# Performance work log

Hardware: AMD Instinct MI355X
Metric: run time of the kernel (lower is better)

The kernel has to match this reference:

```python
import jax, jax.numpy as jnp
import numpy as np

B, T, C = 4, 4096, 512
H, KS = 8, 9
D = C // H
PAD = KS // 2


def setup_inputs() -> dict:
    key = jax.random.key(0)
    ks = jax.random.split(key, 9)
    s = 1.0 / np.sqrt(C)
    return {
        "x": jax.random.normal(ks[0], (B, T, C), jnp.float32),
        "Wq": jax.random.normal(ks[1], (C, C), jnp.float32) * s,
        "bq": jax.random.normal(ks[2], (C,), jnp.float32) * 0.01,
        "Wk": jax.random.normal(ks[3], (C, C), jnp.float32) * s,
        "bk": jax.random.normal(ks[4], (C,), jnp.float32) * 0.01,
        "Wv": jax.random.normal(ks[5], (C, C), jnp.float32) * s,
        "bv": jax.random.normal(ks[6], (C,), jnp.float32) * 0.01,
        "Wo": jax.random.normal(ks[7], (C, C), jnp.float32) * s,
        "bo": jax.random.normal(ks[8], (C,), jnp.float32) * 0.01,
    }


def reference(x, Wq, bq, Wk, bk, Wv, bv, Wo, bo):
    Bx, Tx, Cx = x.shape
    # projections (torch Linear: x @ W.T + b), split heads -> (B,H,T,D)
    q = (x @ Wq.T + bq).reshape(Bx, Tx, H, D).transpose(0, 2, 1, 3)
    k = (x @ Wk.T + bk).reshape(Bx, Tx, H, D).transpose(0, 2, 1, 3)
    v = (x @ Wv.T + bv).reshape(Bx, Tx, H, D).transpose(0, 2, 1, 3)
    # replicate-pad along time (matches F.pad mode='replicate')
    k_pad = jnp.pad(k, ((0, 0), (0, 0), (PAD, PAD), (0, 0)), mode='edge')
    v_pad = jnp.pad(v, ((0, 0), (0, 0), (PAD, PAD), (0, 0)), mode='edge')
    # window gather indices: (T, KS) into padded time axis
    idx = jnp.arange(Tx)[:, None] + jnp.arange(KS)[None, :]
    k_unf = k_pad[:, :, idx, :]  # (B,H,T,KS,D)
    v_unf = v_pad[:, :, idx, :]  # (B,H,T,KS,D)
    scale = 1.0 / np.sqrt(D)
    scores = jnp.einsum('bhtd,bhtkd->bhtk', q, k_unf) * scale  # (B,H,T,KS)
    attn = jax.nn.softmax(scores, axis=-1)
    y = jnp.einsum('bhtk,bhtkd->bhtd', attn, v_unf)  # (B,H,T,D)
    y = y.transpose(0, 2, 1, 3).reshape(Bx, Tx, Cx)
    return y @ Wo.T + bo
```

## Files before the change

kernel.cpp:

```cpp
#include <hip/hip_runtime.h>
#include <hip/hip_bf16.h>

#define B_    4
#define T_    4096
#define C_    512
#define H_    8
#define D_    64
#define KS_   9
#define PAD_  4
#define MTOT  (B_ * T_)
#define PLANE (MTOT * C_)
#define WU    (C_ * C_ / 8)

typedef __bf16 bf16_t;
typedef __bf16 bf16x8 __attribute__((ext_vector_type(8)));
typedef float  f32x4  __attribute__((ext_vector_type(4)));

__global__ __launch_bounds__(256)
void conv_all(const float* __restrict__ Wq, const float* __restrict__ Wk,
              const float* __restrict__ Wv, const float* __restrict__ Wo,
              const float* __restrict__ x,
              bf16_t* __restrict__ Wb, bf16_t* __restrict__ xb) {
  int i = blockIdx.x * 256 + threadIdx.x;
  const float* src;
  bf16_t* dst;
  if (i < 4 * WU) {
    int w = i >> 15;
    const float* W = (w == 0) ? Wq : (w == 1) ? Wk : (w == 2) ? Wv : Wo;
    src = W + (size_t)(i & (WU - 1)) * 8;
    dst = Wb + (size_t)i * 8;
  } else {
    size_t j = (size_t)(i - 4 * WU);
    src = x + j * 8;
    dst = xb + j * 8;
  }
  float4 f0 = ((const float4*)src)[0];
  float4 f1 = ((const float4*)src)[1];
  bf16x8 o;
  o[0] = (bf16_t)f0.x; o[1] = (bf16_t)f0.y; o[2] = (bf16_t)f0.z; o[3] = (bf16_t)f0.w;
  o[4] = (bf16_t)f1.x; o[5] = (bf16_t)f1.y; o[6] = (bf16_t)f1.z; o[7] = (bf16_t)f1.w;
  *(bf16x8*)dst = o;
}

#define BM   256
#define BN   128
#define BK   64
#define NKT  (C_ / BK)
#define ASL  (BM * BK)
#define BSL  (BN * BK)
#define SLOT (ASL + BSL)

#define GLD(srcp, off) __builtin_amdgcn_global_load_lds(                     \
    (const __attribute__((address_space(1))) unsigned int*)(srcp),           \
    (__attribute__((address_space(3))) unsigned int*)(&sm[off]), 16, 0, 0)

template<int MODE>
__global__ __launch_bounds__(512, 2)
void gemm8p(const bf16_t* __restrict__ A, const bf16_t* __restrict__ Bw,
            const float* __restrict__ b0, const float* __restrict__ b1,
            const float* __restrict__ b2, void* __restrict__ Outp) {
  __shared__ __align__(16) bf16_t sm[3 * SLOT];

  constexpr int GX  = (MODE == 0) ? (3 * C_ / BN) : (C_ / BN);
  constexpr int NWG = GX * (MTOT / BM);
  constexpr int CPX = NWG / 8;

  const int ord = blockIdx.y * GX + blockIdx.x;
  const int lg  = (ord & 7) * CPX + (ord >> 3);
  const int n0  = (lg % GX) * BN;
  const int m0  = (lg / GX) * BM;

  const int tid  = threadIdx.x;
  const int lane = tid & 63;
  const int wave = tid >> 6;
  const int wm   = wave >> 1;
  const int wn   = wave & 1;

  const bf16_t* aSrc[4];
  const bf16_t* bSrc[2];
#pragma unroll
  for (int s = 0; s < 4; ++s) {
    int u = s * 512 + tid, r = u >> 3, ch = u & 7;
    int cs = (ch ^ (r & 7)) << 3;
    if constexpr (MODE == 0) {
      aSrc[s] = A + (size_t)(m0 + r) * C_ + cs;
    } else {
      int bb = m0 >> 12, t0 = m0 & (T_ - 1);
      aSrc[s] = A + ((size_t)bb * H_ * T_ + t0 + r) * D_ + cs;
    }
  }
#pragma unroll
  for (int s = 0; s < 2; ++s) {
    int u = s * 512 + tid, r = u >> 3, ch = u & 7;
    int cs = (ch ^ (r & 7)) << 3;
    bSrc[s] = Bw + (size_t)(n0 + r) * C_ + cs;
  }
  constexpr size_t ASTEP = (MODE == 0) ? (size_t)BK : (size_t)T_ * D_;

#pragma unroll
  for (int s = 0; s < 4; ++s) GLD(aSrc[s], (s * 512 + tid) * 8);
#pragma unroll
  for (int s = 0; s < 2; ++s) GLD(bSrc[s], ASL + (s * 512 + tid) * 8);
#pragma unroll
  for (int s = 0; s < 4; ++s) GLD(aSrc[s] + ASTEP, SLOT + (s * 512 + tid) * 8);
#pragma unroll
  for (int s = 0; s < 2; ++s) GLD(bSrc[s] + BK, SLOT + ASL + (s * 512 + tid) * 8);
  asm volatile("s_waitcnt vmcnt(6)" ::: "memory");
  __builtin_amdgcn_s_barrier();

  f32x4 acc[4][4] = {};
  const int lr  = lane & 15;
  const int lq  = lane >> 4;
  const int co0 = ((0 + lq) ^ (lane & 7)) << 3;
  const int co1 = ((4 + lq) ^ (lane & 7)) << 3;

  int rsl = 0;
  for (int kt = 0; kt < NKT; ++kt) {
    const bf16_t* arow = &sm[rsl * SLOT + (wm * 64 + lr) * 64];
    const bf16_t* brow = &sm[rsl * SLOT + ASL + (wn * 64 + lr) * 64];
    const int  wof = ((rsl == 0) ? 2 : rsl - 1) * SLOT;
    const bool st  = (kt + 2 < NKT);
    const size_t ka = (size_t)(kt + 2) * ASTEP;
    const size_t kb = (size_t)(kt + 2) * BK;

    bf16x8 af[4][2], bfr[4][2];

#pragma unroll
    for (int i = 0; i < 4; ++i) {
      af[i][0] = *(const bf16x8*)(arow + i * 1024 + co0);
      af[i][1] = *(const bf16x8*)(arow + i * 1024 + co1);
    }
#pragma unroll
    for (int j = 0; j < 2; ++j) {
      bfr[j][0] = *(const bf16x8*)(brow + j * 1024 + co0);
      bfr[j][1] = *(const bf16x8*)(brow + j * 1024 + co1);
    }
    if (st) {
      GLD(aSrc[0] + ka, wof + (0 * 512 + tid) * 8);
      GLD(aSrc[1] + ka, wof + (1 * 512 + tid) * 8);
      GLD(aSrc[2] + ka, wof + (2 * 512 + tid) * 8);
      GLD(aSrc[3] + ka, wof + (3 * 512 + tid) * 8);
    }
    __builtin_amdgcn_sched_barrier(0);
    __builtin_amdgcn_s_barrier();
    asm volatile("s_waitcnt lgkmcnt(0)" ::: "memory");
    __builtin_amdgcn_sched_barrier(0);
    __builtin_amdgcn_s_setprio(1);
#pragma unroll
    for (int i = 0; i < 4; ++i)
#pragma unroll
      for (int j = 0; j < 2; ++j)
#pragma unroll
        for (int kk = 0; kk < 2; ++kk)
          acc[i][j] = __builtin_amdgcn_mfma_f32_16x16x32_bf16(
              af[i][kk], bfr[j][kk], acc[i][j], 0, 0, 0);
    __builtin_amdgcn_s_setprio(0);
    __builtin_amdgcn_sched_barrier(0);
    __builtin_amdgcn_s_barrier();

#pragma unroll
    for (int j = 2; j < 4; ++j) {
      bfr[j][0] = *(const bf16x8*)(brow + j * 1024 + co0);
      bfr[j][1] = *(const bf16x8*)(brow + j * 1024 + co1);
    }
    if (st) {
      GLD(bSrc[0] + kb, wof + ASL + (0 * 512 + tid) * 8);
      GLD(bSrc[1] + kb, wof + ASL + (1 * 512 + tid) * 8);
    }
    __builtin_amdgcn_sched_barrier(0);
    __builtin_amdgcn_s_barrier();
    asm volatile("s_waitcnt lgkmcnt(0)" ::: "memory");
    __builtin_amdgcn_sched_barrier(0);
    __builtin_amdgcn_s_setprio(1);
#pragma unroll
    for (int i = 0; i < 4; ++i)
#pragma unroll
      for (int j = 2; j < 4; ++j)
#pragma unroll
        for (int kk = 0; kk < 2; ++kk)
          acc[i][j] = __builtin_amdgcn_mfma_f32_16x16x32_bf16(
              af[i][kk], bfr[j][kk], acc[i][j], 0, 0, 0);
    __builtin_amdgcn_s_setprio(0);
    __builtin_amdgcn_sched_barrier(0);
    if (kt < NKT - 2)       asm volatile("s_waitcnt vmcnt(6)" ::: "memory");
    else if (kt == NKT - 2) asm volatile("s_waitcnt vmcnt(0)" ::: "memory");
    __builtin_amdgcn_s_barrier();
    rsl = (rsl == 2) ? 0 : rsl + 1;
  }

  const int cn = lane & 15;
  const int rq = (lane >> 4) << 2;
  if constexpr (MODE == 0) {
    const int z  = n0 >> 9;
    const float* bias = (z == 0) ? b0 : (z == 1) ? b1 : b2;
    const int bb = m0 >> 12;
    const int t0 = m0 & (T_ - 1);
    bf16_t* plane = (bf16_t*)Outp + (size_t)z * PLANE;
#pragma unroll
    for (int j = 0; j < 4; ++j) {
      const int cc  = (n0 & (C_ - 1)) + wn * 64 + j * 16 + cn;
      const int hh  = cc >> 6, dd = cc & 63;
      const float bvv = bias[cc];
      bf16_t* hb = plane + ((size_t)(bb * H_ + hh) * T_) * D_ + dd;
#pragma unroll
      for (int i = 0; i < 4; ++i)
#pragma unroll
        for (int r = 0; r < 4; ++r) {
          const int t = t0 + wm * 64 + i * 16 + rq + r;
          hb[(size_t)t * D_] = (bf16_t)(acc[i][j][r] + bvv);
        }
    }
  } else {
    float* outp = (float*)Outp;
#pragma unroll
    for (int j = 0; j < 4; ++j) {
      const int n = n0 + wn * 64 + j * 16 + cn;
      const float bvv = b0[n];
#pragma unroll
      for (int i = 0; i < 4; ++i)
#pragma unroll
        for (int r = 0; r < 4; ++r) {
          const int m = m0 + wm * 64 + i * 16 + rq + r;
          outp[(size_t)m * C_ + n] = acc[i][j][r] + bvv;
        }
    }
  }
}

__global__ __launch_bounds__(256)
void attn_kernel(const bf16_t* __restrict__ qkv, bf16_t* __restrict__ y) {
  const int tid  = threadIdx.x;
  const int sub  = tid & 7;
  const int tl   = tid >> 3;
  const int t    = blockIdx.x * 32 + tl;
  const int h    = blockIdx.y;
  const int b    = blockIdx.z;

  const size_t pl = (size_t)(b * H_ + h) * T_ * D_;
  const bf16_t* q = qkv + pl;
  const bf16_t* k = qkv + (size_t)PLANE + pl;
  const bf16_t* v = qkv + (size_t)2 * PLANE + pl;
  const int c = sub * 8;

  int tj[KS_];
#pragma unroll
  for (int j = 0; j < KS_; ++j) {
    int tt = t - PAD_ + j;
    tj[j] = tt < 0 ? 0 : (tt >= T_ ? T_ - 1 : tt);
  }

  bf16x8 q8 = *(const bf16x8*)(q + (size_t)t * D_ + c);
  float qf[8];
#pragma unroll
  for (int e = 0; e < 8; ++e) qf[e] = (float)q8[e];

  float s[KS_];
#pragma unroll
  for (int j = 0; j < KS_; ++j) {
    bf16x8 k8 = *(const bf16x8*)(k + (size_t)tj[j] * D_ + c);
    float d0 = 0.f;
#pragma unroll
    for (int e = 0; e < 8; ++e) d0 += qf[e] * (float)k8[e];
    s[j] = d0;
  }

#pragma unroll
  for (int m = 1; m < 8; m <<= 1)
#pragma unroll
    for (int j = 0; j < KS_; ++j) s[j] += __shfl_xor(s[j], m, 8);

  float mx = s[0];
#pragma unroll
  for (int j = 1; j < KS_; ++j) mx = fmaxf(mx, s[j]);
  float w[KS_], sum = 0.f;
#pragma unroll
  for (int j = 0; j < KS_; ++j) {
    w[j] = __expf((s[j] - mx) * 0.125f);
    sum += w[j];
  }
  const float inv = 1.f / sum;
#pragma unroll
  for (int j = 0; j < KS_; ++j) w[j] *= inv;

  float o[8] = {0.f, 0.f, 0.f, 0.f, 0.f, 0.f, 0.f, 0.f};
#pragma unroll
  for (int j = 0; j < KS_; ++j) {
    bf16x8 v8 = *(const bf16x8*)(v + (size_t)tj[j] * D_ + c);
#pragma unroll
    for (int e = 0; e < 8; ++e) o[e] += w[j] * (float)v8[e];
  }
  bf16x8 o8;
#pragma unroll
  for (int e = 0; e < 8; ++e) o8[e] = (bf16_t)o[e];
  *(bf16x8*)(y + pl + (size_t)t * D_ + c) = o8;
}

extern "C" void kernel_launch(void* const* d_in, const int* in_sizes, int n_in,
                              void* d_out, int out_size, void* d_ws, size_t ws_size,
                              hipStream_t stream) {
  const float* x  = (const float*)d_in[0];
  const float* Wq = (const float*)d_in[1];
  const float* bq = (const float*)d_in[2];
  const float* Wk = (const float*)d_in[3];
  const float* bk = (const float*)d_in[4];
  const float* Wv = (const float*)d_in[5];
  const float* bv = (const float*)d_in[6];
  const float* Wo = (const float*)d_in[7];
  const float* bo = (const float*)d_in[8];
  float* out = (float*)d_out;

  bf16_t* Wb  = (bf16_t*)d_ws;
  bf16_t* xb  = Wb + (size_t)4 * C_ * C_;
  bf16_t* qkv = xb + (size_t)PLANE;
  bf16_t* y   = xb;

  conv_all<<<(4 * WU + PLANE / 8) / 256, 256, 0, stream>>>(Wq, Wk, Wv, Wo, x, Wb, xb);
  gemm8p<0><<<dim3(3 * C_ / BN, MTOT / BM), 512, 0, stream>>>(
      xb, Wb, bq, bk, bv, qkv);
  attn_kernel<<<dim3(T_ / 32, H_, B_), 256, 0, stream>>>(qkv, y);
  gemm8p<1><<<dim3(C_ / BN, MTOT / BM), 512, 0, stream>>>(
      y, Wb + (size_t)3 * C_ * C_, bo, nullptr, nullptr, out);
}
```

Baseline: 167.2 us.

## Load GEMM weight fragments directly into registers, bypassing LDS staging

```diff
diff --git a/kernel.cpp b/kernel.cpp
--- a/kernel.cpp
+++ b/kernel.cpp
@@ -47,8 +47,6 @@
 #define BK   64
 #define NKT  (C_ / BK)
 #define ASL  (BM * BK)
-#define BSL  (BN * BK)
-#define SLOT (ASL + BSL)
 
 #define GLD(srcp, off) __builtin_amdgcn_global_load_lds(                     \
     (const __attribute__((address_space(1))) unsigned int*)(srcp),           \
@@ -59,7 +57,7 @@
 void gemm8p(const bf16_t* __restrict__ A, const bf16_t* __restrict__ Bw,
             const float* __restrict__ b0, const float* __restrict__ b1,
             const float* __restrict__ b2, void* __restrict__ Outp) {
-  __shared__ __align__(16) bf16_t sm[3 * SLOT];
+  __shared__ __align__(16) bf16_t sm[3 * ASL];
 
   constexpr int GX  = (MODE == 0) ? (3 * C_ / BN) : (C_ / BN);
   constexpr int NWG = GX * (MTOT / BM);
@@ -75,9 +73,10 @@
   const int wave = tid >> 6;
   const int wm   = wave >> 1;
   const int wn   = wave & 1;
+  const int lr   = lane & 15;
+  const int lq   = lane >> 4;
 
   const bf16_t* aSrc[4];
-  const bf16_t* bSrc[2];
 #pragma unroll
   for (int s = 0; s < 4; ++s) {
     int u = s * 512 + tid, r = u >> 3, ch = u & 7;
@@ -89,103 +88,73 @@
       aSrc[s] = A + ((size_t)bb * H_ * T_ + t0 + r) * D_ + cs;
     }
   }
-#pragma unroll
-  for (int s = 0; s < 2; ++s) {
-    int u = s * 512 + tid, r = u >> 3, ch = u & 7;
-    int cs = (ch ^ (r & 7)) << 3;
-    bSrc[s] = Bw + (size_t)(n0 + r) * C_ + cs;
-  }
   constexpr size_t ASTEP = (MODE == 0) ? (size_t)BK : (size_t)T_ * D_;
 
+  const bf16_t* bBase[4];
+#pragma unroll
+  for (int j = 0; j < 4; ++j)
+    bBase[j] = Bw + (size_t)(n0 + wn * 64 + j * 16 + lr) * C_ + lq * 8;
+
 #pragma unroll
   for (int s = 0; s < 4; ++s) GLD(aSrc[s], (s * 512 + tid) * 8);
 #pragma unroll
-  for (int s = 0; s < 2; ++s) GLD(bSrc[s], ASL + (s * 512 + tid) * 8);
-#pragma unroll
-  for (int s = 0; s < 4; ++s) GLD(aSrc[s] + ASTEP, SLOT + (s * 512 + tid) * 8);
-#pragma unroll
-  for (int s = 0; s < 2; ++s) GLD(bSrc[s] + BK, SLOT + ASL + (s * 512 + tid) * 8);
-  asm volatile("s_waitcnt vmcnt(6)" ::: "memory");
+  for (int s = 0; s < 4; ++s) GLD(aSrc[s] + ASTEP, ASL + (s * 512 + tid) * 8);
+  bf16x8 bfr[2][4][2];
+#pragma unroll
+  for (int j = 0; j < 4; ++j) {
+    bfr[0][j][0] = *(const bf16x8*)(bBase[j]);
+    bfr[0][j][1] = *(const bf16x8*)(bBase[j] + 32);
+  }
+  asm volatile("s_waitcnt vmcnt(12)" ::: "memory");
   __builtin_amdgcn_s_barrier();
 
   f32x4 acc[4][4] = {};
-  const int lr  = lane & 15;
-  const int lq  = lane >> 4;
   const int co0 = ((0 + lq) ^ (lane & 7)) << 3;
   const int co1 = ((4 + lq) ^ (lane & 7)) << 3;
 
-  int rsl = 0;
+#pragma unroll
   for (int kt = 0; kt < NKT; ++kt) {
-    const bf16_t* arow = &sm[rsl * SLOT + (wm * 64 + lr) * 64];
-    const bf16_t* brow = &sm[rsl * SLOT + ASL + (wn * 64 + lr) * 64];
-    const int  wof = ((rsl == 0) ? 2 : rsl - 1) * SLOT;
-    const bool st  = (kt + 2 < NKT);
-    const size_t ka = (size_t)(kt + 2) * ASTEP;
-    const size_t kb = (size_t)(kt + 2) * BK;
-
-    bf16x8 af[4][2], bfr[4][2];
-
+    const int rsl = kt % 3;
+    const int wof = ((kt + 2) % 3) * ASL;
+    const bf16_t* arow = &sm[rsl * ASL + (wm * 64 + lr) * 64];
+
+    bf16x8 af[4][2];
 #pragma unroll
     for (int i = 0; i < 4; ++i) {
       af[i][0] = *(const bf16x8*)(arow + i * 1024 + co0);
       af[i][1] = *(const bf16x8*)(arow + i * 1024 + co1);
     }
-#pragma unroll
-    for (int j = 0; j < 2; ++j) {
-      bfr[j][0] = *(const bf16x8*)(brow + j * 1024 + co0);
-      bfr[j][1] = *(const bf16x8*)(brow + j * 1024 + co1);
-    }
-    if (st) {
-      GLD(aSrc[0] + ka, wof + (0 * 512 + tid) * 8);
-      GLD(aSrc[1] + ka, wof + (1 * 512 + tid) * 8);
-      GLD(aSrc[2] + ka, wof + (2 * 512 + tid) * 8);
-      GLD(aSrc[3] + ka, wof + (3 * 512 + tid) * 8);
+    if (kt + 2 < NKT) {
+#pragma unroll
+      for (int s = 0; s < 4; ++s)
+        GLD(aSrc[s] + (size_t)(kt + 2) * ASTEP, wof + (s * 512 + tid) * 8);
+    }
+    if (kt + 1 < NKT) {
+#pragma unroll
+      for (int j = 0; j < 4; ++j) {
+        bfr[(kt + 1) & 1][j][0] =
+            *(const bf16x8*)(bBase[j] + (kt + 1) * 64);
+        bfr[(kt + 1) & 1][j][1] =
+            *(const bf16x8*)(bBase[j] + (kt + 1) * 64 + 32);
+      }
     }
     __builtin_amdgcn_sched_barrier(0);
-    __builtin_amdgcn_s_barrier();
     asm volatile("s_waitcnt lgkmcnt(0)" ::: "memory");
     __builtin_amdgcn_sched_barrier(0);
     __builtin_amdgcn_s_setprio(1);
 #pragma unroll
     for (int i = 0; i < 4; ++i)
 #pragma unroll
-      for (int j = 0; j < 2; ++j)
+      for (int j = 0; j < 4; ++j)
 #pragma unroll
         for (int kk = 0; kk < 2; ++kk)
           acc[i][j] = __builtin_amdgcn_mfma_f32_16x16x32_bf16(
-              af[i][kk], bfr[j][kk], acc[i][j], 0, 0, 0);
+              af[i][kk], bfr[kt & 1][j][kk], acc[i][j], 0, 0, 0);
     __builtin_amdgcn_s_setprio(0);
     __builtin_amdgcn_sched_barrier(0);
-    __builtin_amdgcn_s_barrier();
-
-#pragma unroll
-    for (int j = 2; j < 4; ++j) {
-      bfr[j][0] = *(const bf16x8*)(brow + j * 1024 + co0);
-      bfr[j][1] = *(const bf16x8*)(brow + j * 1024 + co1);
-    }
-    if (st) {
-      GLD(bSrc[0] + kb, wof + ASL + (0 * 512 + tid) * 8);
-      GLD(bSrc[1] + kb, wof + ASL + (1 * 512 + tid) * 8);
-    }
-    __builtin_amdgcn_sched_barrier(0);
-    __builtin_amdgcn_s_barrier();
-    asm volatile("s_waitcnt lgkmcnt(0)" ::: "memory");
-    __builtin_amdgcn_sched_barrier(0);
-    __builtin_amdgcn_s_setprio(1);
-#pragma unroll
-    for (int i = 0; i < 4; ++i)
-#pragma unroll
-      for (int j = 2; j < 4; ++j)
-#pragma unroll
-        for (int kk = 0; kk < 2; ++kk)
-          acc[i][j] = __builtin_amdgcn_mfma_f32_16x16x32_bf16(
-              af[i][kk], bfr[j][kk], acc[i][j], 0, 0, 0);
-    __builtin_amdgcn_s_setprio(0);
-    __builtin_amdgcn_sched_barrier(0);
-    if (kt < NKT - 2)       asm volatile("s_waitcnt vmcnt(6)" ::: "memory");
-    else if (kt == NKT - 2) asm volatile("s_waitcnt vmcnt(0)" ::: "memory");
-    __builtin_amdgcn_s_barrier();
-    rsl = (rsl == 2) ? 0 : rsl + 1;
+    if (kt + 2 < NKT)      asm volatile("s_waitcnt vmcnt(12)" ::: "memory");
+    else if (kt + 2 == NKT) asm volatile("s_waitcnt vmcnt(8)" ::: "memory");
+    if (kt + 1 < NKT) __builtin_amdgcn_s_barrier();
   }
 
   const int cn = lane & 15;
```

Measured after the change: 207.4 us. +24.1%, slower.
